# Kernel optimization log

Hardware: AMD Instinct MI355X
Metric: run time of the kernel (lower is better)

Reference implementation:

```python
import jax, jax.numpy as jnp
import numpy as np

HEADS = 8
DIM_HEAD = 64
NUM_PATHWAYS = 281
KERNEL = 33
SCALE = DIM_HEAD ** -0.5


def setup_inputs() -> dict:
    key = jax.random.key(0)
    k1, k2, k3 = jax.random.split(key, 3)
    b, n, dim = 1, 16281, 512
    inner = HEADS * DIM_HEAD
    x = jax.random.normal(k1, (b, n, dim), dtype=jnp.float32)
    w_qkv = jax.random.normal(k2, (3 * inner, dim), dtype=jnp.float32) * 0.02
    w_res = jax.random.normal(k3, (HEADS, 1, KERNEL, 1), dtype=jnp.float32) * 0.02
    return {"x": x, "w_qkv": w_qkv, "w_res": w_res}


def _res_conv(v, w_res):
    # v: [b, h, n, d] treated as NCHW; depthwise conv (k,1) along n, groups=h
    pad = KERNEL // 2
    return jax.lax.conv_general_dilated(
        v, w_res, window_strides=(1, 1), padding=((pad, pad), (0, 0)),
        dimension_numbers=("NCHW", "OIHW", "NCHW"), feature_group_count=HEADS)


def reference(x, w_qkv, w_res):
    b, n, dim = x.shape
    m = NUM_PATHWAYS
    qkv = jnp.einsum("bnd,ed->bne", x, w_qkv)  # [b, n, 3*inner]
    q, k, v = jnp.split(qkv, 3, axis=-1)
    def to_heads(t):
        return t.reshape(b, n, HEADS, DIM_HEAD).transpose(0, 2, 1, 3)  # b h n d
    q, k, v = to_heads(q) * SCALE, to_heads(k), to_heads(v)

    q_path, q_hist = q[:, :, :m], q[:, :, m:]
    k_path, k_hist = k[:, :, :m], k[:, :, m:]

    # histology queries attend only to pathway keys (local->global)
    cross_attn_histology = jax.nn.softmax(
        jnp.einsum("bhid,bhjd->bhij", q_hist, k_path), axis=-1)  # [b,h,n-m,m]
    # pathway queries attend to all tokens (global)
    attn_pathways = jnp.einsum("bhid,bhjd->bhij", q_path, k_path)      # [b,h,m,m]
    cross_attn_pathways = jnp.einsum("bhid,bhjd->bhij", q_path, k_hist)  # [b,h,m,n-m]
    attn_pathways_histology = jax.nn.softmax(
        jnp.concatenate([attn_pathways, cross_attn_pathways], axis=-1), axis=-1)

    out_pathways = jnp.einsum("bhij,bhjd->bhid", attn_pathways_histology, v)
    out_histology = jnp.einsum("bhij,bhjd->bhid", cross_attn_histology, v[:, :, :m])
    out = jnp.concatenate([out_pathways, out_histology], axis=2)  # [b,h,n,d]
    out = out + _res_conv(v, w_res)
    return out.transpose(0, 2, 1, 3).reshape(b, n, HEADS * DIM_HEAD)
```

## Files before the change

### kernel.cpp

```cpp
#include <hip/hip_runtime.h>

typedef short short8 __attribute__((ext_vector_type(8)));
typedef float f32x4 __attribute__((ext_vector_type(4)));
typedef unsigned short u16;

#define NTOK 16281
#define NPAD 16384
#define NPATH 281
#define HEADS 8
#define CHUNK 2036
#define KVB 128
#define PATH_QT 5
#define PATH_BLOCKS2 (HEADS * PATH_QT * 8)
#define HIST_QT2 250
#define ATTN_BLOCKS2 (PATH_BLOCKS2 + HEADS * HIST_QT2)

static __device__ __forceinline__ u16 f2bf(float f) {
  unsigned u = __float_as_uint(f);
  u += 0x7FFFu + ((u >> 16) & 1u);
  return (u16)(u >> 16);
}
static __device__ __forceinline__ float bf2f(u16 h) {
  return __uint_as_float(((unsigned)h) << 16);
}
static __device__ __forceinline__ uint2 pack4(float4 v) {
  uint2 o;
  o.x = (unsigned)f2bf(v.x) | ((unsigned)f2bf(v.y) << 16);
  o.y = (unsigned)f2bf(v.z) | ((unsigned)f2bf(v.w) << 16);
  return o;
}

__global__ __launch_bounds__(256) void k_gemm_qkv(const float* __restrict__ x,
                                                  const float* __restrict__ w,
                                                  u16* __restrict__ Qb,
                                                  u16* __restrict__ Kb,
                                                  u16* __restrict__ Vb) {
  __shared__ u16 As[128 * 32];
  __shared__ u16 Bs[128 * 32];
  const int bm = blockIdx.x, bn = blockIdx.y;
  const int t = threadIdx.x;
  const int lane = t & 63, wv = t >> 6;
  const int wr = wv >> 1, wc = wv & 1;
  const int lr = lane & 15, kq = lane >> 4;
  f32x4 acc[4][4] = {};
  for (int ks = 0; ks < 512; ks += 32) {
    for (int c = t; c < 1024; c += 256) {
      int row = c >> 3, c4 = (c & 7) << 2;
      int gr = bm * 128 + row;
      float4 va = {0.f, 0.f, 0.f, 0.f};
      if (gr < NTOK)
        va = *reinterpret_cast<const float4*>(&x[(size_t)gr * 512 + ks + c4]);
      *reinterpret_cast<uint2*>(&As[row * 32 + c4]) = pack4(va);
      float4 vb = *reinterpret_cast<const float4*>(&w[(size_t)(bn * 128 + row) * 512 + ks + c4]);
      *reinterpret_cast<uint2*>(&Bs[row * 32 + c4]) = pack4(vb);
    }
    __syncthreads();
    short8 af[4], bfr[4];
#pragma unroll
    for (int i = 0; i < 4; i++) {
      af[i]  = *reinterpret_cast<const short8*>(&As[(wr * 64 + i * 16 + lr) * 32 + kq * 8]);
      bfr[i] = *reinterpret_cast<const short8*>(&Bs[(wc * 64 + i * 16 + lr) * 32 + kq * 8]);
    }
#pragma unroll
    for (int i = 0; i < 4; i++)
#pragma unroll
      for (int j = 0; j < 4; j++)
        acc[i][j] = __builtin_amdgcn_mfma_f32_16x16x32_bf16(af[i], bfr[j], acc[i][j], 0, 0, 0);
    __syncthreads();
  }
#pragma unroll
  for (int i = 0; i < 4; i++) {
#pragma unroll
    for (int j = 0; j < 4; j++) {
#pragma unroll
      for (int r = 0; r < 4; r++) {
        int row = wr * 64 + i * 16 + kq * 4 + r;
        int col = wc * 64 + j * 16 + lr;
        int n = bm * 128 + row;
        if (n < NTOK) {
          int e = bn * 128 + col;
          int which = e >> 9, h = (e >> 6) & 7, d = e & 63;
          float v = acc[i][j][r];
          size_t off = ((size_t)h * NPAD + n) * 64 + d;
          if (which == 0)      Qb[off] = f2bf(v * 0.125f);
          else if (which == 1) Kb[off] = f2bf(v);
          else                 Vb[off] = f2bf(v);
        }
      }
    }
  }
}

__global__ __launch_bounds__(256) void k_attn_mfma(const u16* __restrict__ Qb,
                                                   const u16* __restrict__ Kb,
                                                   const u16* __restrict__ Vb,
                                                   float* __restrict__ dout,
                                                   float* __restrict__ pp) {
  __shared__ u16 Kt[KVB * 64];
  __shared__ u16 Vt[64 * KVB];
  __shared__ u16 Pt[4][16 * KVB];

  const int b = blockIdx.x, t = threadIdx.x;
  const int lane = t & 63, wq = t >> 6;
  const int c = lane & 15, g = lane >> 4;
  int h, q0, k0, k1, qlim;
  bool path;
  if (b < PATH_BLOCKS2) {
    path = true;
    int qt = (b >> 3) % PATH_QT;
    h = b / (8 * PATH_QT);
    q0 = qt * 64;
    k0 = (b & 7) * CHUNK;
    k1 = min(k0 + CHUNK, NTOK);
    qlim = NPATH;
  } else {
    path = false;
    int bb = b - PATH_BLOCKS2;
    h = bb / HIST_QT2;
    q0 = NPATH + (bb % HIST_QT2) * 64;
    k0 = 0; k1 = NPATH;
    qlim = NTOK;
  }
  const int q = q0 + wq * 16 + c;
  short8 qf0 = {}, qf1 = {};
  if (q < qlim) {
    qf0 = *reinterpret_cast<const short8*>(&Qb[((size_t)h * NPAD + q) * 64 + g * 8]);
    qf1 = *reinterpret_cast<const short8*>(&Qb[((size_t)h * NPAD + q) * 64 + 32 + g * 8]);
  }
  float m_run[4], l_run[4];
#pragma unroll
  for (int r = 0; r < 4; r++) { m_run[r] = -1e30f; l_run[r] = 0.f; }
  f32x4 o[4] = {};

  for (int j0 = k0; j0 < k1; j0 += KVB) {
    const int jn = min(KVB, k1 - j0);
    __syncthreads();
#pragma unroll
    for (int it = 0; it < 4; it++) {
      int i = t + it * 256;
      int row = i >> 3, cc = i & 7;
      uint4 vv = {0u, 0u, 0u, 0u};
      if (row < jn)
        vv = *reinterpret_cast<const uint4*>(&Kb[((size_t)h * NPAD + j0 + row) * 64 + cc * 8]);
      *reinterpret_cast<uint4*>(&Kt[row * 64 + ((cc ^ (row & 7)) << 3)]) = vv;
    }
#pragma unroll
    for (int it = 0; it < 4; it++) {
      int i = t + it * 256;
      int key = i >> 3, dc = i & 7;
      uint4 vv = {0u, 0u, 0u, 0u};
      if (key < jn)
        vv = *reinterpret_cast<const uint4*>(&Vb[((size_t)h * NPAD + j0 + key) * 64 + dc * 8]);
      const u16* pv = reinterpret_cast<const u16*>(&vv);
#pragma unroll
      for (int u = 0; u < 8; u++) {
        int d = dc * 8 + u;
        Vt[d * KVB + (key ^ ((d & 7) << 3))] = pv[u];
      }
    }
    __syncthreads();
    f32x4 s[8];
#pragma unroll
    for (int kt = 0; kt < 8; kt++) {
      int key = kt * 16 + c;
      int swz = (key & 7) << 3;
      short8 bk0 = *reinterpret_cast<const short8*>(&Kt[key * 64 + ((g * 8) ^ swz)]);
      short8 bk1 = *reinterpret_cast<const short8*>(&Kt[key * 64 + ((32 + g * 8) ^ swz)]);
      f32x4 z = {0.f, 0.f, 0.f, 0.f};
      z = __builtin_amdgcn_mfma_f32_16x16x32_bf16(qf0, bk0, z, 0, 0, 0);
      s[kt] = __builtin_amdgcn_mfma_f32_16x16x32_bf16(qf1, bk1, z, 0, 0, 0);
    }
    if (jn < KVB) {
#pragma unroll
      for (int kt = 0; kt < 8; kt++)
        if (kt * 16 + c >= jn) {
          s[kt][0] = -1e30f; s[kt][1] = -1e30f; s[kt][2] = -1e30f; s[kt][3] = -1e30f;
        }
    }
    float fac[4];
#pragma unroll
    for (int r = 0; r < 4; r++) {
      float m2 = s[0][r];
#pragma unroll
      for (int kt = 1; kt < 8; kt++) m2 = fmaxf(m2, s[kt][r]);
#pragma unroll
      for (int msk = 1; msk < 16; msk <<= 1) m2 = fmaxf(m2, __shfl_xor(m2, msk, 64));
      float mnew = fmaxf(m_run[r], m2);
      fac[r] = __expf(m_run[r] - mnew);
      m_run[r] = mnew;
    }
#pragma unroll
    for (int r = 0; r < 4; r++) {
      float ps = 0.f;
#pragma unroll
      for (int kt = 0; kt < 8; kt++) {
        float e = __expf(s[kt][r] - m_run[r]);
        s[kt][r] = e;
        ps += e;
      }
#pragma unroll
      for (int msk = 1; msk < 16; msk <<= 1) ps += __shfl_xor(ps, msk, 64);
      l_run[r] = l_run[r] * fac[r] + ps;
    }
#pragma unroll
    for (int dt = 0; dt < 4; dt++) {
#pragma unroll
      for (int r = 0; r < 4; r++) o[dt][r] *= fac[r];
    }
#pragma unroll
    for (int r = 0; r < 4; r++) {
      int qrow = g * 4 + r;
      int swz = (qrow & 7) << 3;
#pragma unroll
      for (int kt = 0; kt < 8; kt++)
        Pt[wq][qrow * KVB + ((kt * 16 + c) ^ swz)] = f2bf(s[kt][r]);
    }
#pragma unroll
    for (int ks = 0; ks < 4; ks++) {
      short8 pa = *reinterpret_cast<const short8*>(
          &Pt[wq][c * KVB + ((ks * 32 + g * 8) ^ ((c & 7) << 3))]);
#pragma unroll
      for (int dt = 0; dt < 4; dt++) {
        int d = dt * 16 + c;
        short8 bv = *reinterpret_cast<const short8*>(
            &Vt[d * KVB + ((ks * 32 + g * 8) ^ ((d & 7) << 3))]);
        o[dt] = __builtin_amdgcn_mfma_f32_16x16x32_bf16(pa, bv, o[dt], 0, 0, 0);
      }
    }
  }

  if (path) {
    int kc = b & 7;
#pragma unroll
    for (int r = 0; r < 4; r++) {
      int qp = q0 + wq * 16 + g * 4 + r;
      if (qp < NPATH) {
        float* base = pp + ((size_t)(h * 8 + kc) * NPATH + qp) * 66;
#pragma unroll
        for (int dt = 0; dt < 4; dt++) base[dt * 16 + c] = o[dt][r];
        if (c == 0) { base[64] = m_run[r]; base[65] = l_run[r]; }
      }
    }
  } else {
#pragma unroll
    for (int r = 0; r < 4; r++) {
      int qn = q0 + wq * 16 + g * 4 + r;
      float inv = 1.f / l_run[r];
#pragma unroll
      for (int dt = 0; dt < 4; dt++)
        dout[(size_t)qn * 512 + h * 64 + dt * 16 + c] = o[dt][r] * inv;
    }
  }
}

__global__ void k_combine(const float* __restrict__ pp, float* __restrict__ dout) {
  const int b = blockIdx.x;
  const int h = b / NPATH, q = b % NPATH;
  const int d = threadIdx.x;
  const float* base0 = pp + ((size_t)(h * 8) * NPATH + q) * 66;
  const size_t cs = (size_t)NPATH * 66;
  float m = -1e30f;
  for (int c = 0; c < 8; c++) m = fmaxf(m, base0[c * cs + 64]);
  float l = 0.f, o = 0.f;
  for (int c = 0; c < 8; c++) {
    const float* base = base0 + c * cs;
    float sc = __expf(base[64] - m);
    l += sc * base[65];
    o += sc * base[d];
  }
  dout[(size_t)q * 512 + h * 64 + d] = o / l;
}

__global__ __launch_bounds__(256) void k_conv(const u16* __restrict__ Vb,
                                              const float* __restrict__ wres,
                                              float* __restrict__ dout) {
  __shared__ float Vs[96][64];
  __shared__ float wr[33];
  const int b = blockIdx.x;
  const int h = b / 255, n0 = (b % 255) * 64;
  const int t = threadIdx.x;
  if (t < 33) wr[t] = wres[h * 33 + t];
  for (int i = t; i < 96 * 64; i += 256) {
    int rr = i >> 6, dd = i & 63;
    int n = n0 - 16 + rr;
    Vs[rr][dd] = (n >= 0 && n < NTOK) ? bf2f(Vb[((size_t)h * NPAD + n) * 64 + dd]) : 0.f;
  }
  __syncthreads();
  const int d = t & 63, ns = t >> 6;
  for (int i = 0; i < 16; i++) {
    int nn = ns * 16 + i;
    int n = n0 + nn;
    if (n < NTOK) {
      float s = 0.f;
#pragma unroll
      for (int u = 0; u < 33; u++) s += Vs[nn + u][d] * wr[u];
      dout[(size_t)n * 512 + h * 64 + d] += s;
    }
  }
}

extern "C" void kernel_launch(void* const* d_in, const int* in_sizes, int n_in,
                              void* d_out, int out_size, void* d_ws, size_t ws_size,
                              hipStream_t stream) {
  const float* x    = (const float*)d_in[0];
  const float* wqkv = (const float*)d_in[1];
  const float* wres = (const float*)d_in[2];
  float* out = (float*)d_out;
  char* ws = (char*)d_ws;
  const size_t NEED = 55079424;
  if (ws_size < NEED) return;
  u16*   Qb = (u16*)(ws + 0);
  u16*   Kb = (u16*)(ws + 16777216);
  u16*   Vb = (u16*)(ws + 33554432);
  float* pp = (float*)(ws + 50331648);

  hipLaunchKernelGGL(k_gemm_qkv, dim3(128, 12), dim3(256), 0, stream, x, wqkv, Qb, Kb, Vb);
  hipLaunchKernelGGL(k_attn_mfma, dim3(ATTN_BLOCKS2), dim3(256), 0, stream, Qb, Kb, Vb, out, pp);
  hipLaunchKernelGGL(k_combine, dim3(HEADS * NPATH), dim3(64), 0, stream, pp, out);
  hipLaunchKernelGGL(k_conv, dim3(HEADS * 255), dim3(256), 0, stream, Vb, wres, out);
}
```

Baseline: 234.8 us.

## Pre-transpose V into global memory and drop LDS V staging in attention

Adds a kernel that writes a d-major transposed copy of V, so attention can load its V MFMA fragments straight from global memory instead of scattering V into shared memory one element at a time each KV tile. A zero-pad kernel clears the padded token rows, since V tiles are no longer masked per key. The residual conv now runs first and writes the output directly, and attention and combine accumulate into it. The partials buffer reuses V's workspace region. The trade-offs are two extra launches and strided, less coalesced global reads of V, which rely on cache hits.

```diff
diff --git a/kernel.cpp b/kernel.cpp
--- a/kernel.cpp
+++ b/kernel.cpp
@@ -14,6 +14,8 @@
 #define PATH_BLOCKS2 (HEADS * PATH_QT * 8)
 #define HIST_QT2 250
 #define ATTN_BLOCKS2 (PATH_BLOCKS2 + HEADS * HIST_QT2)
+#define NPADROWS (NPAD - NTOK)
+#define ZERON (HEADS * NPADROWS * 64)
 
 static __device__ __forceinline__ u16 f2bf(float f) {
   unsigned u = __float_as_uint(f);
@@ -28,6 +30,18 @@
   o.x = (unsigned)f2bf(v.x) | ((unsigned)f2bf(v.y) << 16);
   o.y = (unsigned)f2bf(v.z) | ((unsigned)f2bf(v.w) << 16);
   return o;
+}
+
+__global__ __launch_bounds__(256) void k_zeropad(u16* __restrict__ Qb,
+                                                 u16* __restrict__ Kb,
+                                                 u16* __restrict__ Vb) {
+  int i = blockIdx.x * 256 + threadIdx.x;
+  if (i >= ZERON) return;
+  int d = i & 63;
+  int rr = (i >> 6) % NPADROWS;
+  int h = i / (NPADROWS * 64);
+  size_t off = ((size_t)h * NPAD + NTOK + rr) * 64 + d;
+  Qb[off] = 0; Kb[off] = 0; Vb[off] = 0;
 }
 
 __global__ __launch_bounds__(256) void k_gemm_qkv(const float* __restrict__ x,
@@ -91,13 +105,41 @@
   }
 }
 
+__global__ __launch_bounds__(256) void k_vt(const u16* __restrict__ Vb,
+                                            u16* __restrict__ VbT) {
+  __shared__ u16 T[128 * 64];
+  const int h = blockIdx.x, kt = blockIdx.y;
+  const int t = threadIdx.x;
+#pragma unroll
+  for (int it = 0; it < 4; it++) {
+    int i = t + it * 256;
+    int row = i >> 3, dc = i & 7;
+    uint4 vv = *reinterpret_cast<const uint4*>(
+        &Vb[((size_t)h * NPAD + kt * 128 + row) * 64 + dc * 8]);
+    *reinterpret_cast<uint4*>(&T[row * 64 + ((dc ^ (row & 7)) << 3)]) = vv;
+  }
+  __syncthreads();
+  const int d = t & 63, wv = t >> 6;
+#pragma unroll
+  for (int it = 0; it < 4; it++) {
+    int kc = wv + it * 4;
+    u16 g[8];
+#pragma unroll
+    for (int u = 0; u < 8; u++) {
+      int key = kc * 8 + u;
+      g[u] = T[key * 64 + ((((d >> 3) ^ (key & 7)) << 3) | (d & 7))];
+    }
+    *reinterpret_cast<uint4*>(&VbT[((size_t)h * 64 + d) * NPAD + kt * 128 + kc * 8]) =
+        *reinterpret_cast<uint4*>(g);
+  }
+}
+
 __global__ __launch_bounds__(256) void k_attn_mfma(const u16* __restrict__ Qb,
                                                    const u16* __restrict__ Kb,
-                                                   const u16* __restrict__ Vb,
+                                                   const u16* __restrict__ VbT,
                                                    float* __restrict__ dout,
                                                    float* __restrict__ pp) {
   __shared__ u16 Kt[KVB * 64];
-  __shared__ u16 Vt[64 * KVB];
   __shared__ u16 Pt[4][16 * KVB];
 
   const int b = blockIdx.x, t = threadIdx.x;
@@ -127,6 +169,7 @@
     qf0 = *reinterpret_cast<const short8*>(&Qb[((size_t)h * NPAD + q) * 64 + g * 8]);
     qf1 = *reinterpret_cast<const short8*>(&Qb[((size_t)h * NPAD + q) * 64 + 32 + g * 8]);
   }
+  const u16* vt = VbT + (size_t)h * 64 * NPAD;
   float m_run[4], l_run[4];
 #pragma unroll
   for (int r = 0; r < 4; r++) { m_run[r] = -1e30f; l_run[r] = 0.f; }
@@ -143,20 +186,6 @@
       if (row < jn)
         vv = *reinterpret_cast<const uint4*>(&Kb[((size_t)h * NPAD + j0 + row) * 64 + cc * 8]);
       *reinterpret_cast<uint4*>(&Kt[row * 64 + ((cc ^ (row & 7)) << 3)]) = vv;
-    }
-#pragma unroll
-    for (int it = 0; it < 4; it++) {
-      int i = t + it * 256;
-      int key = i >> 3, dc = i & 7;
-      uint4 vv = {0u, 0u, 0u, 0u};
-      if (key < jn)
-        vv = *reinterpret_cast<const uint4*>(&Vb[((size_t)h * NPAD + j0 + key) * 64 + dc * 8]);
-      const u16* pv = reinterpret_cast<const u16*>(&vv);
-#pragma unroll
-      for (int u = 0; u < 8; u++) {
-        int d = dc * 8 + u;
-        Vt[d * KVB + (key ^ ((d & 7) << 3))] = pv[u];
-      }
     }
     __syncthreads();
     f32x4 s[8];
@@ -221,9 +250,8 @@
           &Pt[wq][c * KVB + ((ks * 32 + g * 8) ^ ((c & 7) << 3))]);
 #pragma unroll
       for (int dt = 0; dt < 4; dt++) {
-        int d = dt * 16 + c;
         short8 bv = *reinterpret_cast<const short8*>(
-            &Vt[d * KVB + ((ks * 32 + g * 8) ^ ((d & 7) << 3))]);
+            &vt[(size_t)(dt * 16 + c) * NPAD + j0 + ks * 32 + g * 8]);
         o[dt] = __builtin_amdgcn_mfma_f32_16x16x32_bf16(pa, bv, o[dt], 0, 0, 0);
       }
     }
@@ -248,7 +276,7 @@
       float inv = 1.f / l_run[r];
 #pragma unroll
       for (int dt = 0; dt < 4; dt++)
-        dout[(size_t)qn * 512 + h * 64 + dt * 16 + c] = o[dt][r] * inv;
+        dout[(size_t)qn * 512 + h * 64 + dt * 16 + c] += o[dt][r] * inv;
     }
   }
 }
@@ -268,7 +296,7 @@
     l += sc * base[65];
     o += sc * base[d];
   }
-  dout[(size_t)q * 512 + h * 64 + d] = o / l;
+  dout[(size_t)q * 512 + h * 64 + d] += o / l;
 }
 
 __global__ __launch_bounds__(256) void k_conv(const u16* __restrict__ Vb,
@@ -294,7 +322,7 @@
       float s = 0.f;
 #pragma unroll
       for (int u = 0; u < 33; u++) s += Vs[nn + u][d] * wr[u];
-      dout[(size_t)n * 512 + h * 64 + d] += s;
+      dout[(size_t)n * 512 + h * 64 + d] = s;
     }
   }
 }
@@ -307,15 +335,18 @@
   const float* wres = (const float*)d_in[2];
   float* out = (float*)d_out;
   char* ws = (char*)d_ws;
-  const size_t NEED = 55079424;
+  const size_t NEED = 67108864;
   if (ws_size < NEED) return;
-  u16*   Qb = (u16*)(ws + 0);
-  u16*   Kb = (u16*)(ws + 16777216);
-  u16*   Vb = (u16*)(ws + 33554432);
-  float* pp = (float*)(ws + 50331648);
-
+  u16*   Qb  = (u16*)(ws + 0);
+  u16*   Kb  = (u16*)(ws + 16777216);
+  u16*   Vb  = (u16*)(ws + 33554432);
+  u16*   VbT = (u16*)(ws + 50331648);
+  float* pp  = (float*)(ws + 33554432);
+
+  hipLaunchKernelGGL(k_zeropad, dim3((ZERON + 255) / 256), dim3(256), 0, stream, Qb, Kb, Vb);
   hipLaunchKernelGGL(k_gemm_qkv, dim3(128, 12), dim3(256), 0, stream, x, wqkv, Qb, Kb, Vb);
-  hipLaunchKernelGGL(k_attn_mfma, dim3(ATTN_BLOCKS2), dim3(256), 0, stream, Qb, Kb, Vb, out, pp);
+  hipLaunchKernelGGL(k_conv, dim3(HEADS * 255), dim3(256), 0, stream, Vb, wres, out);
+  hipLaunchKernelGGL(k_vt, dim3(HEADS, 128), dim3(256), 0, stream, Vb, VbT);
+  hipLaunchKernelGGL(k_attn_mfma, dim3(ATTN_BLOCKS2), dim3(256), 0, stream, Qb, Kb, VbT, out, pp);
   hipLaunchKernelGGL(k_combine, dim3(HEADS * NPATH), dim3(64), 0, stream, pp, out);
-  hipLaunchKernelGGL(k_conv, dim3(HEADS * 255), dim3(256), 0, stream, Vb, wres, out);
-}
+}
```

Result: slower. 253.3 us (+7.9%).
